# Kernel tuning notes

Measured on AMD Instinct MI355X. Metric: run time of the kernel, lower is better.

Reference implementation:

```python
import jax, jax.numpy as jnp
import numpy as np

B, K, D, L = 512, 800, 512, 500000

def setup_inputs() -> dict:
    key = jax.random.key(0)
    k1, k2, k3, k4 = jax.random.split(key, 4)
    stdv = 1.0 / np.sqrt(D)
    embed = jax.random.normal(k1, (B, D), dtype=jnp.float32)
    shortlist = jax.random.randint(k2, (B, K), 0, L, dtype=jnp.int32)
    sp_weight = jax.random.uniform(k3, (L, D), dtype=jnp.float32, minval=-stdv, maxval=stdv)
    sp_bias = jax.random.uniform(k4, (L, 1), dtype=jnp.float32, minval=-stdv, maxval=stdv)
    return {"embed": embed, "shortlist": shortlist, "sp_weight": sp_weight, "sp_bias": sp_bias}

def reference(embed, shortlist, sp_weight, sp_bias):
    # gather shortlist weight rows: [B, K, D]
    short_w = sp_weight[shortlist]
    # batched dot product: [B, K]
    out = jnp.einsum('bd,bkd->bk', embed, short_w)
    # gather bias rows [B, K, 1] -> add
    out = out + sp_bias[shortlist, 0]
    return out
```

## Files before the change

### kernel.cpp

```cpp
#include <hip/hip_runtime.h>


#define DDIM 512
#define KTOT 800
#define KCHUNKS 4
#define KPB (KTOT / KCHUNKS)

__global__ __launch_bounds__(256, 4)
void sparse_linear_kernel(const float* __restrict__ embed,
                          const int* __restrict__ shortlist,
                          const float* __restrict__ sp_weight,
                          const float* __restrict__ sp_bias,
                          float* __restrict__ out) {
    const int b     = blockIdx.x;
    const int kbase = blockIdx.y * KPB;
    const int wave  = threadIdx.x >> 6;
    const int lane  = threadIdx.x & 63;

    const float4* e4 = (const float4*)(embed + (size_t)b * DDIM);
    const float4 e0 = e4[lane];
    const float4 e1 = e4[64 + lane];

    const int* sl_row = shortlist + (size_t)b * KTOT;
    float* out_row = out + (size_t)b * KTOT;

    for (int k = kbase + wave * 2; k < kbase + KPB; k += 8) {
        const int ia = sl_row[k];
        const int ib = sl_row[k + 1];
        const float4* wa = (const float4*)(sp_weight + (size_t)ia * DDIM);
        const float4* wb = (const float4*)(sp_weight + (size_t)ib * DDIM);
        const float4 a0 = wa[lane];
        const float4 a1 = wa[64 + lane];
        const float4 b0 = wb[lane];
        const float4 b1 = wb[64 + lane];

        float pa = a0.x * e0.x + a0.y * e0.y + a0.z * e0.z + a0.w * e0.w
                 + a1.x * e1.x + a1.y * e1.y + a1.z * e1.z + a1.w * e1.w;
        float pb = b0.x * e0.x + b0.y * e0.y + b0.z * e0.z + b0.w * e0.w
                 + b1.x * e1.x + b1.y * e1.y + b1.z * e1.z + b1.w * e1.w;

        #pragma unroll
        for (int off = 32; off > 0; off >>= 1) {
            pa += __shfl_down(pa, off, 64);
            pb += __shfl_down(pb, off, 64);
        }

        if (lane == 0) {
            out_row[k]     = pa + sp_bias[ia];
            out_row[k + 1] = pb + sp_bias[ib];
        }
    }
}

extern "C" void kernel_launch(void* const* d_in, const int* in_sizes, int n_in,
                              void* d_out, int out_size, void* d_ws, size_t ws_size,
                              hipStream_t stream) {
    const float* embed     = (const float*)d_in[0];
    const int*   shortlist = (const int*)d_in[1];
    const float* sp_weight = (const float*)d_in[2];
    const float* sp_bias   = (const float*)d_in[3];
    float* out = (float*)d_out;

    dim3 grid(512, KCHUNKS);
    dim3 block(256);
    hipLaunchKernelGGL(sparse_linear_kernel, grid, block, 0, stream,
                       embed, shortlist, sp_weight, sp_bias, out);
}
```

Measured before the change: 1.225 ms.

## Process eight gathered rows per wave with prefetched indices and vector loads

Each wave now handles eight shortlist rows per iteration instead of two, issuing sixteen float4 gathers at once to raise memory-level parallelism. Shortlist indices are loaded as int4 vectors and the next iteration's indices are prefetched. Bias loads and output stores are spread across lanes 0-7. The chunk count changes from 4 to 5 so each block covers 160 columns in 5 fixed iterations. The extra live float4 registers raise VGPR pressure, which may conflict with the launch-bounds occupancy target.

Result: no change. 1.212 ms (-1.1%).

```diff
diff --git a/kernel.cpp b/kernel.cpp
--- a/kernel.cpp
+++ b/kernel.cpp
@@ -3,8 +3,15 @@
 
 #define DDIM 512
 #define KTOT 800
-#define KCHUNKS 4
+#define KCHUNKS 5
 #define KPB (KTOT / KCHUNKS)
+#define KITER 5
+
+__device__ __forceinline__ float dot8(const float4 a0, const float4 a1,
+                                      const float4 e0, const float4 e1) {
+    return a0.x * e0.x + a0.y * e0.y + a0.z * e0.z + a0.w * e0.w
+         + a1.x * e1.x + a1.y * e1.y + a1.z * e1.z + a1.w * e1.w;
+}
 
 __global__ __launch_bounds__(256, 4)
 void sparse_linear_kernel(const float* __restrict__ embed,
@@ -14,41 +21,94 @@
                           float* __restrict__ out) {
     const int b     = blockIdx.x;
     const int kbase = blockIdx.y * KPB;
-    const int wave  = threadIdx.x >> 6;
-    const int lane  = threadIdx.x & 63;
+    const int wave  = (int)(threadIdx.x >> 6);
+    const int lane  = (int)(threadIdx.x & 63);
 
     const float4* e4 = (const float4*)(embed + (size_t)b * DDIM);
     const float4 e0 = e4[lane];
     const float4 e1 = e4[64 + lane];
 
-    const int* sl_row = shortlist + (size_t)b * KTOT;
-    float* out_row = out + (size_t)b * KTOT;
+    const int* sl_row  = shortlist + (size_t)b * KTOT;
+    float*     out_row = out + (size_t)b * KTOT;
 
-    for (int k = kbase + wave * 2; k < kbase + KPB; k += 8) {
-        const int ia = sl_row[k];
-        const int ib = sl_row[k + 1];
-        const float4* wa = (const float4*)(sp_weight + (size_t)ia * DDIM);
-        const float4* wb = (const float4*)(sp_weight + (size_t)ib * DDIM);
-        const float4 a0 = wa[lane];
-        const float4 a1 = wa[64 + lane];
-        const float4 b0 = wb[lane];
-        const float4 b1 = wb[64 + lane];
+    const int k0 = kbase + wave * 8;
+    int4 ia = *(const int4*)(sl_row + k0);
+    int4 ib = *(const int4*)(sl_row + k0 + 4);
 
-        float pa = a0.x * e0.x + a0.y * e0.y + a0.z * e0.z + a0.w * e0.w
-                 + a1.x * e1.x + a1.y * e1.y + a1.z * e1.z + a1.w * e1.w;
-        float pb = b0.x * e0.x + b0.y * e0.y + b0.z * e0.z + b0.w * e0.w
-                 + b1.x * e1.x + b1.y * e1.y + b1.z * e1.z + b1.w * e1.w;
+    #pragma unroll 1
+    for (int i = 0; i < KITER; ++i) {
+        const int k = k0 + i * 32;
+
+        const float4* w0 = (const float4*)(sp_weight + (size_t)ia.x * DDIM);
+        const float4* w1 = (const float4*)(sp_weight + (size_t)ia.y * DDIM);
+        const float4* w2 = (const float4*)(sp_weight + (size_t)ia.z * DDIM);
+        const float4* w3 = (const float4*)(sp_weight + (size_t)ia.w * DDIM);
+        const float4* w4 = (const float4*)(sp_weight + (size_t)ib.x * DDIM);
+        const float4* w5 = (const float4*)(sp_weight + (size_t)ib.y * DDIM);
+        const float4* w6 = (const float4*)(sp_weight + (size_t)ib.z * DDIM);
+        const float4* w7 = (const float4*)(sp_weight + (size_t)ib.w * DDIM);
+
+        const float4 a00 = w0[lane], a01 = w0[64 + lane];
+        const float4 a10 = w1[lane], a11 = w1[64 + lane];
+        const float4 a20 = w2[lane], a21 = w2[64 + lane];
+        const float4 a30 = w3[lane], a31 = w3[64 + lane];
+        const float4 a40 = w4[lane], a41 = w4[64 + lane];
+        const float4 a50 = w5[lane], a51 = w5[64 + lane];
+        const float4 a60 = w6[lane], a61 = w6[64 + lane];
+        const float4 a70 = w7[lane], a71 = w7[64 + lane];
+
+        int myidx = ia.x;
+        myidx = (lane == 1) ? ia.y : myidx;
+        myidx = (lane == 2) ? ia.z : myidx;
+        myidx = (lane == 3) ? ia.w : myidx;
+        myidx = (lane == 4) ? ib.x : myidx;
+        myidx = (lane == 5) ? ib.y : myidx;
+        myidx = (lane == 6) ? ib.z : myidx;
+        myidx = (lane == 7) ? ib.w : myidx;
+        float mybias = 0.0f;
+        if (lane < 8) mybias = sp_bias[myidx];
+
+        int4 na = ia, nb = ib;
+        if (i < KITER - 1) {
+            na = *(const int4*)(sl_row + k + 32);
+            nb = *(const int4*)(sl_row + k + 36);
+        }
+
+        float p0 = dot8(a00, a01, e0, e1);
+        float p1 = dot8(a10, a11, e0, e1);
+        float p2 = dot8(a20, a21, e0, e1);
+        float p3 = dot8(a30, a31, e0, e1);
+        float p4 = dot8(a40, a41, e0, e1);
+        float p5 = dot8(a50, a51, e0, e1);
+        float p6 = dot8(a60, a61, e0, e1);
+        float p7 = dot8(a70, a71, e0, e1);
 
         #pragma unroll
-        for (int off = 32; off > 0; off >>= 1) {
-            pa += __shfl_down(pa, off, 64);
-            pb += __shfl_down(pb, off, 64);
+        for (int m = 1; m < 64; m <<= 1) {
+            p0 += __shfl_xor(p0, m, 64);
+            p1 += __shfl_xor(p1, m, 64);
+            p2 += __shfl_xor(p2, m, 64);
+            p3 += __shfl_xor(p3, m, 64);
+            p4 += __shfl_xor(p4, m, 64);
+            p5 += __shfl_xor(p5, m, 64);
+            p6 += __shfl_xor(p6, m, 64);
+            p7 += __shfl_xor(p7, m, 64);
         }
 
-        if (lane == 0) {
-            out_row[k]     = pa + sp_bias[ia];
-            out_row[k + 1] = pb + sp_bias[ib];
+        if (lane < 8) {
+            float myp = p0;
+            myp = (lane == 1) ? p1 : myp;
+            myp = (lane == 2) ? p2 : myp;
+            myp = (lane == 3) ? p3 : myp;
+            myp = (lane == 4) ? p4 : myp;
+            myp = (lane == 5) ? p5 : myp;
+            myp = (lane == 6) ? p6 : myp;
+            myp = (lane == 7) ? p7 : myp;
+            out_row[k + lane] = myp + mybias;
         }
+
+        ia = na;
+        ib = nb;
     }
 }
 
```
